# Performance work log

Measured on AMD Instinct MI355X. Metric: run time of the kernel, lower is better.

Reference implementation:

```python
import jax, jax.numpy as jnp
import numpy as np

B, N, D = 32, 1024, 256  # batch, nodes, feature dim (input=hidden=output=256)


def setup_inputs() -> dict:
    key = jax.random.key(0)
    ks = jax.random.split(key, 9)
    x = jax.random.normal(ks[0], (B, N, D), dtype=jnp.float32)
    # binary node mask (multiplied in, so float dtype)
    mask = (jax.random.uniform(ks[1], (B, N)) > 0.2).astype(jnp.float32)
    # dense nonneg adjacency; row sums > 0 almost surely
    adj = jax.random.uniform(ks[2], (B, N, N), dtype=jnp.float32)
    s = 1.0 / np.sqrt(D)
    W0 = jax.random.normal(ks[3], (D, D), dtype=jnp.float32) * s
    b0 = jnp.zeros((D,), dtype=jnp.float32)
    W1 = jax.random.normal(ks[4], (D, D), dtype=jnp.float32) * s
    b1 = jnp.zeros((D,), dtype=jnp.float32)
    W2 = jax.random.normal(ks[5], (D, D), dtype=jnp.float32) * s
    b2 = jnp.zeros((D,), dtype=jnp.float32)
    return {"x": x, "mask": mask, "adj": adj,
            "W0": W0, "b0": b0, "W1": W1, "b1": b1, "W2": W2, "b2": b2}


def reference(x, mask, adj, W0, b0, W1, b1, W2, b2):
    # D_hat = diag(1/rowsum(adj)) with inf -> 0; diag matmul == row-wise scale
    deg = jnp.sum(adj, axis=-1)                                   # [B,N]
    dinv = jnp.where(deg != 0, 1.0 / jnp.where(deg != 0, deg, 1.0), 0.0)
    adj_n = adj * dinv[..., None]                                 # [B,N,N]
    xm = mask[..., None]                                          # [B,N,1]
    # dropout is identity in eval mode
    for W, b in ((W0, b0), (W1, b1), (W2, b2)):
        x = jnp.matmul(x, W.T) + b                                # linear
        x = jnp.einsum('bnm,bmd->bnd', adj_n, x)                  # aggregate
        x = x * xm                                                # mask
        x = jax.nn.gelu(x, approximate=False)                     # exact gelu (torch F.gelu)
    return x
```

## Files before the change

kernel.cpp:

```cpp
#include <hip/hip_runtime.h>
#include <stdint.h>


typedef __attribute__((ext_vector_type(8))) short short8;
typedef __attribute__((ext_vector_type(4))) float f32x4;

__device__ __forceinline__ uint16_t f2bf(float f) {
  uint32_t u = __float_as_uint(f);
  u += 0x7FFF + ((u >> 16) & 1);
  return (uint16_t)(u >> 16);
}
__device__ __forceinline__ float bf2f(uint16_t h) {
  return __uint_as_float(((uint32_t)h) << 16);
}
__device__ __forceinline__ float gelu_exact(float v) {
  return 0.5f * v * (1.0f + erff(v * 0.70710678118654752f));
}
__device__ __forceinline__ f32x4 mfma16(short8 a, short8 b, f32x4 c) {
  return __builtin_amdgcn_mfma_f32_16x16x32_bf16(a, b, c, 0, 0, 0);
}

#define GLD16(gsrc, ldst) __builtin_amdgcn_global_load_lds(                    \
    (const __attribute__((address_space(1))) void*)(gsrc),                     \
    (__attribute__((address_space(3))) void*)(ldst), 16, 0, 0)

__global__ void k_cast(const float* __restrict__ src, uint16_t* __restrict__ h,
                       int n4) {
  int i = blockIdx.x * blockDim.x + threadIdx.x;
  if (i >= n4) return;
  const float4 v = ((const float4*)src)[i];
  float vv[4] = {v.x, v.y, v.z, v.w};
  ushort4 hh;
  uint16_t* hp = (uint16_t*)&hh;
#pragma unroll
  for (int e = 0; e < 4; ++e) hp[e] = f2bf(vv[e]);
  ((ushort4*)h)[i] = hh;
}

__global__ void k_split(const float* __restrict__ src, uint16_t* __restrict__ h,
                        uint16_t* __restrict__ l, int n4) {
  int i = blockIdx.x * blockDim.x + threadIdx.x;
  if (i >= n4) return;
  const float4 v = ((const float4*)src)[i];
  float vv[4] = {v.x, v.y, v.z, v.w};
  ushort4 hh, ll;
  uint16_t* hp = (uint16_t*)&hh;
  uint16_t* lp = (uint16_t*)&ll;
#pragma unroll
  for (int e = 0; e < 4; ++e) {
    uint16_t hb = f2bf(vv[e]);
    hp[e] = hb;
    lp[e] = f2bf(vv[e] - bf2f(hb));
  }
  ((ushort4*)h)[i] = hh;
  ((ushort4*)l)[i] = ll;
}

__global__ void k_norm_adj(const float* __restrict__ adj, uint16_t* __restrict__ An) {
  const int r = blockIdx.x;
  const int t = threadIdx.x;
  const float* row = adj + (size_t)r * 1024;
  const float4 v = *(const float4*)(row + t * 4);
  float s = v.x + v.y + v.z + v.w;
#pragma unroll
  for (int off = 32; off; off >>= 1) s += __shfl_down(s, off);
  __shared__ float ws[4];
  if ((t & 63) == 0) ws[t >> 6] = s;
  __syncthreads();
  const float deg = ws[0] + ws[1] + ws[2] + ws[3];
  const float dinv = (deg != 0.f) ? 1.f / deg : 0.f;
  ushort4 o;
  uint16_t* op = (uint16_t*)&o;
  float vv[4] = {v.x, v.y, v.z, v.w};
#pragma unroll
  for (int e = 0; e < 4; ++e) op[e] = f2bf(vv[e] * dinv);
  const int b = r >> 10, node = r & 1023;
  const int mb = node >> 7, rr = node & 127;
  const int kt = t >> 3, ko = (t * 4) & 31;
  const size_t oo = (size_t)(b * 8 + mb) * 131072 + kt * 4096 + rr * 32 + ko;
  *(ushort4*)(An + oo) = o;
}

__global__ __launch_bounds__(256) void k_linear(
    const uint16_t* __restrict__ Xh,
    const uint16_t* __restrict__ Wh, const uint16_t* __restrict__ Wl,
    const float* __restrict__ bias,
    uint16_t* __restrict__ Yth) {
  __shared__ __align__(16) uint8_t smem[24576];
  const int tid = threadIdx.x;
  const int lane = tid & 63;
  const int wave = tid >> 6;
  const int wr = wave >> 1, wc = wave & 1;
  const int m0 = blockIdx.x * 128;
  const int n0 = blockIdx.y * 128;
  const int lm = lane & 15, g = lane >> 4;
  const int srow = lane >> 2;
  const int skof = (lane & 3) * 8;

  f32x4 acc[4][4] = {};

  for (int kt = 0; kt < 8; ++kt) {
    const int k0 = kt * 32;
    __syncthreads();
#pragma unroll
    for (int j = 0; j < 6; ++j) {
      const int c = j * 4 + wave;
      const int sub = c & 7, which = c >> 3;
      const int row = sub * 16 + srow;
      const uint16_t* src;
      if (which == 0)      src = Xh + (size_t)(m0 + row) * 256 + k0 + skof;
      else if (which == 1) src = Wh + (size_t)(n0 + row) * 256 + k0 + skof;
      else                 src = Wl + (size_t)(n0 + row) * 256 + k0 + skof;
      GLD16(src, smem + c * 1024);
    }
    asm volatile("s_waitcnt vmcnt(0)" ::: "memory");
    __syncthreads();

    const uint8_t* Ahs = smem;
    const uint8_t* Bhs = smem + 8192;
    const uint8_t* Bls = smem + 16384;
    short8 ah[4], bh[4], bl[4];
#pragma unroll
    for (int f = 0; f < 4; ++f) {
      ah[f] = *(const short8*)(Ahs + (wr * 64 + f * 16 + lm) * 64 + g * 16);
      bh[f] = *(const short8*)(Bhs + (wc * 64 + f * 16 + lm) * 64 + g * 16);
      bl[f] = *(const short8*)(Bls + (wc * 64 + f * 16 + lm) * 64 + g * 16);
    }
#pragma unroll
    for (int fm = 0; fm < 4; ++fm)
#pragma unroll
      for (int fn = 0; fn < 4; ++fn) {
        acc[fm][fn] = mfma16(ah[fm], bh[fn], acc[fm][fn]);
        acc[fm][fn] = mfma16(ah[fm], bl[fn], acc[fm][fn]);
      }
  }

#pragma unroll
  for (int fn = 0; fn < 4; ++fn) {
    const int n = n0 + wc * 64 + fn * 16 + lm;
    const float bv = bias[n];
#pragma unroll
    for (int fm = 0; fm < 4; ++fm) {
      const int mg = m0 + wr * 64 + fm * 16 + g * 4;
      const int bb = mg >> 10, node = mg & 1023;
      const int kt = node >> 5, ko = node & 31;
      ushort4 hh;
      uint16_t* hp = (uint16_t*)&hh;
#pragma unroll
      for (int e = 0; e < 4; ++e) hp[e] = f2bf(acc[fm][fn][e] + bv);
      const size_t o = ((size_t)(bb * 32 + kt) * 256 + n) * 32 + ko;
      *(ushort4*)(Yth + o) = hh;
    }
  }
}

#define STAGE(T, SSL) {                                                        \
    _Pragma("unroll")                                                          \
    for (int j = 0; j < 4; ++j) {                                              \
      const int c = w * 4 + j;                                                 \
      const uint16_t* src = (c < 8)                                            \
          ? aStep + (size_t)(T) * 4096 + c * 512                               \
          : yStep + (size_t)(T) * 8192 + (c - 8) * 512;                        \
      GLD16(src, smem + (SSL) + c * 1024);                                     \
    }                                                                          \
  }

template <bool LAST>
__global__ __launch_bounds__(256, 2) void k_agg(
    const uint16_t* __restrict__ An,
    const uint16_t* __restrict__ Yth,
    const float* __restrict__ mask,
    uint16_t* __restrict__ Xh,
    float* __restrict__ out) {
  __shared__ __align__(16) uint8_t smem[65536];
  const int tid = threadIdx.x;
  const int lane = tid & 63;
  const int w = tid >> 6;
  const int wm = w >> 1, wn = w & 1;
  const int id = blockIdx.x;
  const int swz = (id & 7) * 64 + (id >> 3);
  const int b = swz >> 4;
  const int rest = swz & 15;
  const int mb = rest >> 1;
  const int nh = rest & 1;
  const int lm = lane & 15, g = lane >> 4;

  const uint16_t* aStep = An + (size_t)(b * 8 + mb) * 131072 + lane * 8;
  const uint16_t* yStep = Yth + (size_t)b * 262144 + nh * 4096 + lane * 8;

  const int aoff = (wm * 64 + lm) * 64 + g * 16;
  const int boff = 8192 + (wn * 64 + lm) * 64 + g * 16;

  f32x4 acc[4][4] = {};

  STAGE(0, 0);
  STAGE(1, 16384);
  STAGE(2, 32768);

  int csl = 0, ssl = 49152;
#pragma unroll 1
  for (int t = 0; t < 32; ++t) {
    if (t < 30)      { asm volatile("s_waitcnt vmcnt(8)" ::: "memory"); }
    else if (t == 30){ asm volatile("s_waitcnt vmcnt(4)" ::: "memory"); }
    else             { asm volatile("s_waitcnt vmcnt(0)" ::: "memory"); }
    __builtin_amdgcn_s_barrier();
    __builtin_amdgcn_sched_barrier(0);
    if (t < 29) { STAGE(t + 3, ssl); }
    __builtin_amdgcn_sched_barrier(0);

    const uint8_t* sb = smem + csl;
    short8 af[4];
#pragma unroll
    for (int f = 0; f < 4; ++f) af[f] = *(const short8*)(sb + aoff + f * 1024);
    __builtin_amdgcn_s_setprio(1);
#pragma unroll
    for (int fn = 0; fn < 4; ++fn) {
      const short8 hf = *(const short8*)(sb + boff + fn * 1024);
#pragma unroll
      for (int fm = 0; fm < 4; ++fm)
        acc[fm][fn] = mfma16(af[fm], hf, acc[fm][fn]);
    }
    __builtin_amdgcn_s_setprio(0);

    csl += 16384; if (csl == 65536) csl = 0;
    ssl += 16384; if (ssl == 65536) ssl = 0;
  }

  const float* mk_b = mask + b * 1024;
#pragma unroll
  for (int fm = 0; fm < 4; ++fm) {
    const int m = mb * 128 + wm * 64 + fm * 16 + g * 4;
    float mk[4];
#pragma unroll
    for (int e = 0; e < 4; ++e) mk[e] = mk_b[m + e];
#pragma unroll
    for (int fn = 0; fn < 4; ++fn) {
      const int n = nh * 128 + wn * 64 + fn * 16 + lm;
#pragma unroll
      for (int e = 0; e < 4; ++e) {
        const float v = gelu_exact(acc[fm][fn][e] * mk[e]);
        const size_t o = ((size_t)(b * 1024 + m + e)) * 256 + n;
        if (LAST) {
          out[o] = v;
        } else {
          Xh[o] = f2bf(v);
        }
      }
    }
  }
}

extern "C" void kernel_launch(void* const* d_in, const int* in_sizes, int n_in,
                              void* d_out, int out_size, void* d_ws, size_t ws_size,
                              hipStream_t stream) {
  const float* x    = (const float*)d_in[0];
  const float* mask = (const float*)d_in[1];
  const float* adj  = (const float*)d_in[2];
  const float* W[3]  = {(const float*)d_in[3], (const float*)d_in[5], (const float*)d_in[7]};
  const float* bs[3] = {(const float*)d_in[4], (const float*)d_in[6], (const float*)d_in[8]};

  uint8_t* ws = (uint8_t*)d_ws;
  uint16_t* An  = (uint16_t*)(ws);
  uint16_t* Xh  = (uint16_t*)(ws + 67108864);
  uint16_t* Yth = (uint16_t*)(ws + 83886080);
  uint16_t* Wh  = (uint16_t*)(ws + 100663296);
  uint16_t* Wl  = (uint16_t*)(ws + 101056512);

  k_cast<<<dim3(8192), 256, 0, stream>>>(x, Xh, 2097152);
  for (int i = 0; i < 3; ++i)
    k_split<<<dim3(64), 256, 0, stream>>>(W[i], Wh + i * 65536, Wl + i * 65536, 16384);
  k_norm_adj<<<dim3(32768), 256, 0, stream>>>(adj, An);

  for (int l = 0; l < 3; ++l) {
    k_linear<<<dim3(256, 2), 256, 0, stream>>>(Xh, Wh + l * 65536, Wl + l * 65536,
                                               bs[l], Yth);
    if (l < 2)
      k_agg<false><<<dim3(512), 256, 0, stream>>>(An, Yth, mask, Xh, nullptr);
    else
      k_agg<true><<<dim3(512), 256, 0, stream>>>(An, Yth, mask, nullptr,
                                                 (float*)d_out);
  }
}
```

Before: 184.7 us.

## Restructure aggregation into per-wave private LDS pipeline with register A-fragments

```diff
diff --git a/kernel.cpp b/kernel.cpp
--- a/kernel.cpp
+++ b/kernel.cpp
@@ -37,10 +37,12 @@
   ((ushort4*)h)[i] = hh;
 }
 
-__global__ void k_split(const float* __restrict__ src, uint16_t* __restrict__ h,
-                        uint16_t* __restrict__ l, int n4) {
-  int i = blockIdx.x * blockDim.x + threadIdx.x;
-  if (i >= n4) return;
+__global__ void k_split3(const float* __restrict__ s0, const float* __restrict__ s1,
+                         const float* __restrict__ s2,
+                         uint16_t* __restrict__ h, uint16_t* __restrict__ l) {
+  const int blk = blockIdx.x >> 6;
+  const int i = (blockIdx.x & 63) * 256 + threadIdx.x;
+  const float* src = (blk == 0) ? s0 : (blk == 1) ? s1 : s2;
   const float4 v = ((const float4*)src)[i];
   float vv[4] = {v.x, v.y, v.z, v.w};
   ushort4 hh, ll;
@@ -52,8 +54,8 @@
     hp[e] = hb;
     lp[e] = f2bf(vv[e] - bf2f(hb));
   }
-  ((ushort4*)h)[i] = hh;
-  ((ushort4*)l)[i] = ll;
+  ((ushort4*)(h + blk * 65536))[i] = hh;
+  ((ushort4*)(l + blk * 65536))[i] = ll;
 }
 
 __global__ void k_norm_adj(const float* __restrict__ adj, uint16_t* __restrict__ An) {
@@ -154,15 +156,49 @@
   }
 }
 
-#define STAGE(T, SSL) {                                                        \
+#define ASTEP(AF) {                                                            \
     _Pragma("unroll")                                                          \
-    for (int j = 0; j < 4; ++j) {                                              \
-      const int c = w * 4 + j;                                                 \
-      const uint16_t* src = (c < 8)                                            \
-          ? aStep + (size_t)(T) * 4096 + c * 512                               \
-          : yStep + (size_t)(T) * 8192 + (c - 8) * 512;                        \
-      GLD16(src, smem + (SSL) + c * 1024);                                     \
+    for (int j = 0; j < 4; ++j)                                                \
+      GLD16(yBase + (size_t)ks * 8192 + j * 512 + lane * 8,                    \
+            myl + ssl + j * 1024);                                             \
+    __builtin_amdgcn_sched_barrier(0);                                         \
+    asm volatile("s_waitcnt vmcnt(12)" ::: "memory");                          \
+    __builtin_amdgcn_sched_barrier(0);                                         \
+    {                                                                          \
+      const uint8_t* sb = myl + csl;                                           \
+      __builtin_amdgcn_s_setprio(1);                                           \
+      _Pragma("unroll")                                                        \
+      for (int fn = 0; fn < 4; ++fn) {                                         \
+        const short8 hf = *(const short8*)(sb + hoff + fn * 1024);             \
+        _Pragma("unroll")                                                      \
+        for (int fm = 0; fm < 4; ++fm)                                         \
+          acc[fm][fn] = mfma16(AF[fm], hf, acc[fm][fn]);                       \
+      }                                                                        \
+      __builtin_amdgcn_s_setprio(0);                                           \
     }                                                                          \
+    __builtin_amdgcn_sched_barrier(0);                                         \
+    _Pragma("unroll")                                                          \
+    for (int f = 0; f < 4; ++f)                                                \
+      AF[f] = *(const short8*)(aBase + (size_t)ks * 4096 + f * 512);           \
+    ks++;                                                                      \
+    csl += 4096; if (csl == 12288) csl = 0;                                    \
+    ssl += 4096; if (ssl == 12288) ssl = 0;                                    \
+  }
+
+#define ATAIL(AF, VM) {                                                        \
+    asm volatile("s_waitcnt vmcnt(" #VM ")" ::: "memory");                     \
+    __builtin_amdgcn_sched_barrier(0);                                         \
+    const uint8_t* sb = myl + csl;                                             \
+    __builtin_amdgcn_s_setprio(1);                                             \
+    _Pragma("unroll")                                                          \
+    for (int fn = 0; fn < 4; ++fn) {                                           \
+      const short8 hf = *(const short8*)(sb + hoff + fn * 1024);               \
+      _Pragma("unroll")                                                        \
+      for (int fm = 0; fm < 4; ++fm)                                           \
+        acc[fm][fn] = mfma16(AF[fm], hf, acc[fm][fn]);                         \
+    }                                                                          \
+    __builtin_amdgcn_s_setprio(0);                                             \
+    csl += 4096; if (csl == 12288) csl = 0;                                    \
   }
 
 template <bool LAST>
@@ -172,7 +208,7 @@
     const float* __restrict__ mask,
     uint16_t* __restrict__ Xh,
     float* __restrict__ out) {
-  __shared__ __align__(16) uint8_t smem[65536];
+  __shared__ __align__(16) uint8_t smem[49152];
   const int tid = threadIdx.x;
   const int lane = tid & 63;
   const int w = tid >> 6;
@@ -185,46 +221,39 @@
   const int nh = rest & 1;
   const int lm = lane & 15, g = lane >> 4;
 
-  const uint16_t* aStep = An + (size_t)(b * 8 + mb) * 131072 + lane * 8;
-  const uint16_t* yStep = Yth + (size_t)b * 262144 + nh * 4096 + lane * 8;
-
-  const int aoff = (wm * 64 + lm) * 64 + g * 16;
-  const int boff = 8192 + (wn * 64 + lm) * 64 + g * 16;
+  uint8_t* myl = smem + w * 12288;
+  const uint16_t* aBase = An + (size_t)(b * 8 + mb) * 131072
+                             + (wm * 64 + lm) * 32 + g * 8;
+  const uint16_t* yBase = Yth + (size_t)b * 262144 + (nh * 128 + wn * 64) * 32;
+  const int hoff = lm * 64 + g * 16;
 
   f32x4 acc[4][4] = {};
-
-  STAGE(0, 0);
-  STAGE(1, 16384);
-  STAGE(2, 32768);
-
-  int csl = 0, ssl = 49152;
+  short8 afA[4], afB[4];
+
+#pragma unroll
+  for (int j = 0; j < 4; ++j)
+    GLD16(yBase + j * 512 + lane * 8, myl + j * 1024);
+  __builtin_amdgcn_sched_barrier(0);
+#pragma unroll
+  for (int f = 0; f < 4; ++f) afA[f] = *(const short8*)(aBase + f * 512);
+  __builtin_amdgcn_sched_barrier(0);
+#pragma unroll
+  for (int j = 0; j < 4; ++j)
+    GLD16(yBase + 8192 + j * 512 + lane * 8, myl + 4096 + j * 1024);
+  __builtin_amdgcn_sched_barrier(0);
+#pragma unroll
+  for (int f = 0; f < 4; ++f) afB[f] = *(const short8*)(aBase + 4096 + f * 512);
+  __builtin_amdgcn_sched_barrier(0);
+
+  int ks = 2;
+  int csl = 0, ssl = 8192;
 #pragma unroll 1
-  for (int t = 0; t < 32; ++t) {
-    if (t < 30)      { asm volatile("s_waitcnt vmcnt(8)" ::: "memory"); }
-    else if (t == 30){ asm volatile("s_waitcnt vmcnt(4)" ::: "memory"); }
-    else             { asm volatile("s_waitcnt vmcnt(0)" ::: "memory"); }
-    __builtin_amdgcn_s_barrier();
-    __builtin_amdgcn_sched_barrier(0);
-    if (t < 29) { STAGE(t + 3, ssl); }
-    __builtin_amdgcn_sched_barrier(0);
-
-    const uint8_t* sb = smem + csl;
-    short8 af[4];
-#pragma unroll
-    for (int f = 0; f < 4; ++f) af[f] = *(const short8*)(sb + aoff + f * 1024);
-    __builtin_amdgcn_s_setprio(1);
-#pragma unroll
-    for (int fn = 0; fn < 4; ++fn) {
-      const short8 hf = *(const short8*)(sb + boff + fn * 1024);
-#pragma unroll
-      for (int fm = 0; fm < 4; ++fm)
-        acc[fm][fn] = mfma16(af[fm], hf, acc[fm][fn]);
-    }
-    __builtin_amdgcn_s_setprio(0);
-
-    csl += 16384; if (csl == 65536) csl = 0;
-    ssl += 16384; if (ssl == 65536) ssl = 0;
-  }
+  for (int tp = 0; tp < 15; ++tp) {
+    ASTEP(afA);
+    ASTEP(afB);
+  }
+  ATAIL(afA, 8);
+  ATAIL(afB, 0);
 
   const float* mk_b = mask + b * 1024;
 #pragma unroll
@@ -267,8 +296,7 @@
   uint16_t* Wl  = (uint16_t*)(ws + 101056512);
 
   k_cast<<<dim3(8192), 256, 0, stream>>>(x, Xh, 2097152);
-  for (int i = 0; i < 3; ++i)
-    k_split<<<dim3(64), 256, 0, stream>>>(W[i], Wh + i * 65536, Wl + i * 65536, 16384);
+  k_split3<<<dim3(192), 256, 0, stream>>>(W[0], W[1], W[2], Wh, Wl);
   k_norm_adj<<<dim3(32768), 256, 0, stream>>>(adj, An);
 
   for (int l = 0; l < 3; ++l) {
```

Result: slower. 193.4 us (+4.7%).
